# Optimization experiments

Hardware: AMD Instinct MI355X
Metric: run time of the kernel (lower is better)

The kernel has to match this reference:

```python
import jax, jax.numpy as jnp
import numpy as np

GAMMA = 1.0

def setup_inputs() -> dict:
    key = jax.random.key(0)
    kx, ky = jax.random.split(key)
    X = jax.random.normal(kx, (8192, 64), dtype=jnp.float32)
    Y = jax.random.normal(ky, (8192, 64), dtype=jnp.float32)
    return {"X": X, "Y": Y}

def reference(X, Y):
    x2 = jnp.sum(X * X, axis=-1)            # (n,)
    y2 = jnp.sum(Y * Y, axis=-1)            # (m,)
    xy = X @ Y.T                            # (n, m)
    dist2 = x2[:, None] + y2[None, :] - 2.0 * xy
    dist2 = jnp.maximum(dist2, 0.0)         # numerical guard
    return jnp.exp(-GAMMA * dist2)
```

## Files before the change

### kernel.cpp

```cpp
#include <hip/hip_runtime.h>

typedef __attribute__((ext_vector_type(8))) short          short8_t;
typedef __attribute__((ext_vector_type(8))) unsigned short ushort8_t;
typedef __attribute__((ext_vector_type(4))) float          floatx4;

constexpr int N_ROWS = 8192;
constexpr int DIM    = 64;
constexpr int PANEL  = 128 * DIM;

__device__ __forceinline__ unsigned short bf16_rne(float f) {
    unsigned int u = __float_as_uint(f);
    u += 0x7FFFu + ((u >> 16) & 1u);
    return (unsigned short)(u >> 16);
}

__global__ void __launch_bounds__(256)
split_norms_kernel(const float* __restrict__ X, const float* __restrict__ Y,
                   float* __restrict__ x2, float* __restrict__ y2,
                   unsigned short* __restrict__ Xs, unsigned short* __restrict__ Ys) {
    const int t  = blockIdx.x * 256 + threadIdx.x;
    const int r  = t >> 1;
    const int h  = t & 1;
    const int p  = r >> 7;
    const int rl = r & 127;
    const int g  = rl >> 4;
    const int li = rl & 15;
    const size_t pb = (size_t)p * (2 * PANEL);

    const float4* xr = reinterpret_cast<const float4*>(X + (size_t)r * DIM + h * 32);
    const float4* yr = reinterpret_cast<const float4*>(Y + (size_t)r * DIM + h * 32);

    float sx = 0.f, sy = 0.f;
#pragma unroll
    for (int c = 0; c < 4; ++c) {
        const int off = ((g * 2 + h) * 64 + c * 16 + li) * 8;
        float f[8];
        ushort8_t hi, lo;

        *reinterpret_cast<float4*>(&f[0]) = xr[2 * c];
        *reinterpret_cast<float4*>(&f[4]) = xr[2 * c + 1];
#pragma unroll
        for (int e = 0; e < 8; ++e) {
            sx = fmaf(f[e], f[e], sx);
            unsigned short hh = bf16_rne(f[e]);
            hi[e] = hh;
            lo[e] = bf16_rne(f[e] - __uint_as_float((unsigned int)hh << 16));
        }
        *reinterpret_cast<ushort8_t*>(&Xs[pb + off])         = hi;
        *reinterpret_cast<ushort8_t*>(&Xs[pb + PANEL + off]) = lo;

        *reinterpret_cast<float4*>(&f[0]) = yr[2 * c];
        *reinterpret_cast<float4*>(&f[4]) = yr[2 * c + 1];
#pragma unroll
        for (int e = 0; e < 8; ++e) {
            sy = fmaf(f[e], f[e], sy);
            unsigned short hh = bf16_rne(f[e]);
            hi[e] = hh;
            lo[e] = bf16_rne(f[e] - __uint_as_float((unsigned int)hh << 16));
        }
        *reinterpret_cast<ushort8_t*>(&Ys[pb + off])         = hi;
        *reinterpret_cast<ushort8_t*>(&Ys[pb + PANEL + off]) = lo;
    }
    sx += __shfl_xor(sx, 1);
    sy += __shfl_xor(sy, 1);
    if (h == 0) { x2[r] = sx; y2[r] = sy; }
}

__global__ void __launch_bounds__(64)
rbf_mfma_kernel(const unsigned short* __restrict__ Xs,
                const unsigned short* __restrict__ Ys,
                const float* __restrict__ x2, const float* __restrict__ y2,
                float* __restrict__ out) {
    const int lane = threadIdx.x;
    const int row0 = blockIdx.y * 64;
    const int col0 = blockIdx.x * 64;
    const unsigned short* Xp = Xs + (size_t)(blockIdx.y >> 1) * (2 * PANEL);
    const unsigned short* Yp = Ys + (size_t)(blockIdx.x >> 1) * (2 * PANEL);
    const int gx0 = (blockIdx.y & 1) * 4;
    const int gy0 = (blockIdx.x & 1) * 4;

    floatx4 acc[4][4] = {};

#define GF(P, hl, g, ks)                                                       \
    (*reinterpret_cast<const short8_t*>(                                       \
        (P) + (hl) * PANEL + (((g) * 2 + (ks)) * 64 + lane) * 8))

#pragma unroll
    for (int ks = 0; ks < 2; ++ks) {
        short8_t aH[4], bH[4], aL[4], bL[4];
#pragma unroll
        for (int mi = 0; mi < 4; ++mi) aH[mi] = GF(Xp, 0, gx0 + mi, ks);
#pragma unroll
        for (int ni = 0; ni < 4; ++ni) bH[ni] = GF(Yp, 0, gy0 + ni, ks);
#pragma unroll
        for (int mi = 0; mi < 4; ++mi)
#pragma unroll
            for (int ni = 0; ni < 4; ++ni)
                acc[mi][ni] = __builtin_amdgcn_mfma_f32_16x16x32_bf16(
                    bH[ni], aH[mi], acc[mi][ni], 0, 0, 0);
#pragma unroll
        for (int ni = 0; ni < 4; ++ni) bL[ni] = GF(Yp, 1, gy0 + ni, ks);
#pragma unroll
        for (int mi = 0; mi < 4; ++mi)
#pragma unroll
            for (int ni = 0; ni < 4; ++ni)
                acc[mi][ni] = __builtin_amdgcn_mfma_f32_16x16x32_bf16(
                    bL[ni], aH[mi], acc[mi][ni], 0, 0, 0);
#pragma unroll
        for (int mi = 0; mi < 4; ++mi) aL[mi] = GF(Xp, 1, gx0 + mi, ks);
#pragma unroll
        for (int mi = 0; mi < 4; ++mi)
#pragma unroll
            for (int ni = 0; ni < 4; ++ni)
                acc[mi][ni] = __builtin_amdgcn_mfma_f32_16x16x32_bf16(
                    bH[ni], aL[mi], acc[mi][ni], 0, 0, 0);
    }
#undef GF

    const int li = lane & 15;
    const int lg = lane >> 4;
    const int orow = row0 + li;
    const int ocol = col0 + lg * 4;
#pragma unroll
    for (int mi = 0; mi < 4; ++mi) {
        const float xs = x2[orow + mi * 16];
        float* obase = out + (size_t)(orow + mi * 16) * N_ROWS + ocol;
#pragma unroll
        for (int ni = 0; ni < 4; ++ni) {
            const float4 yv = *reinterpret_cast<const float4*>(&y2[ocol + ni * 16]);
            float4 o;
            o.x = __expf(-fmaxf(fmaf(-2.f, acc[mi][ni][0], xs + yv.x), 0.f));
            o.y = __expf(-fmaxf(fmaf(-2.f, acc[mi][ni][1], xs + yv.y), 0.f));
            o.z = __expf(-fmaxf(fmaf(-2.f, acc[mi][ni][2], xs + yv.z), 0.f));
            o.w = __expf(-fmaxf(fmaf(-2.f, acc[mi][ni][3], xs + yv.w), 0.f));
            *reinterpret_cast<float4*>(obase + ni * 16) = o;
        }
    }
}

extern "C" void kernel_launch(void* const* d_in, const int* in_sizes, int n_in,
                              void* d_out, int out_size, void* d_ws, size_t ws_size,
                              hipStream_t stream) {
    const float* X = (const float*)d_in[0];
    const float* Y = (const float*)d_in[1];
    float* out = (float*)d_out;

    float* x2 = (float*)d_ws;
    float* y2 = x2 + N_ROWS;
    unsigned short* Xs = (unsigned short*)(y2 + N_ROWS);
    unsigned short* Ys = Xs + (N_ROWS / 128) * 2 * PANEL;

    split_norms_kernel<<<(2 * N_ROWS) / 256, 256, 0, stream>>>(X, Y, x2, y2, Xs, Ys);

    dim3 grid(N_ROWS / 64, N_ROWS / 64);
    rbf_mfma_kernel<<<grid, 64, 0, stream>>>(Xs, Ys, x2, y2, out);
}
```

Baseline: 73.60 us.

## Persistent 256-thread blocks with register-resident X and LDS-transposed coalesced stores

Replaces the 16K single-wave blocks with 256 persistent blocks of four waves. Each wave keeps its 64-row X fragments in registers and loops over 16 column chunks of 64. Accumulators are staged through a per-wave swizzled LDS buffer so each output row is written as 256 contiguous bytes rather than scattered 16-byte pieces. This targets launch overhead, repeated X loads and store coalescing on a write-bound 256MB output. The trade-off is fewer blocks, which may limit latency hiding, plus LDS traffic and serialized per-chunk phases.

```diff
diff --git a/kernel.cpp b/kernel.cpp
--- a/kernel.cpp
+++ b/kernel.cpp
@@ -66,74 +66,98 @@
     if (h == 0) { x2[r] = sx; y2[r] = sy; }
 }
 
-__global__ void __launch_bounds__(64)
+__global__ void __launch_bounds__(256, 2)
 rbf_mfma_kernel(const unsigned short* __restrict__ Xs,
                 const unsigned short* __restrict__ Ys,
                 const float* __restrict__ x2, const float* __restrict__ y2,
                 float* __restrict__ out) {
-    const int lane = threadIdx.x;
-    const int row0 = blockIdx.y * 64;
-    const int col0 = blockIdx.x * 64;
-    const unsigned short* Xp = Xs + (size_t)(blockIdx.y >> 1) * (2 * PANEL);
-    const unsigned short* Yp = Ys + (size_t)(blockIdx.x >> 1) * (2 * PANEL);
-    const int gx0 = (blockIdx.y & 1) * 4;
-    const int gy0 = (blockIdx.x & 1) * 4;
+    __shared__ float4 Rbuf[4][1024];
 
-    floatx4 acc[4][4] = {};
+    const int tid  = threadIdx.x;
+    const int lane = tid & 63;
+    const int w    = tid >> 6;
+    const int li   = lane & 15;
+    const int lg   = lane >> 4;
 
-#define GF(P, hl, g, ks)                                                       \
-    (*reinterpret_cast<const short8_t*>(                                       \
-        (P) + (hl) * PANEL + (((g) * 2 + (ks)) * 64 + lane) * 8))
+    const int band = blockIdx.x & 31;
+    const int cq   = blockIdx.x >> 5;
+    const int row0 = band * 256 + w * 64;
+    const int colbase = cq * 1024;
+
+    short8_t aH[4][2], aL[4][2];
+    const int gx0 = row0 >> 4;
+#pragma unroll
+    for (int gx = 0; gx < 4; ++gx) {
+        const int gabs = gx0 + gx;
+        const unsigned short* base = Xs + (size_t)(gabs >> 3) * (2 * PANEL);
+        const int g = gabs & 7;
+#pragma unroll
+        for (int ks = 0; ks < 2; ++ks) {
+            const int off = ((g * 2 + ks) * 64 + lane) * 8;
+            aH[gx][ks] = *reinterpret_cast<const short8_t*>(base + off);
+            aL[gx][ks] = *reinterpret_cast<const short8_t*>(base + PANEL + off);
+        }
+    }
+
+    for (int ch = 0; ch < 16; ++ch) {
+        const int c0 = colbase + ch * 64;
+
+        short8_t bH[4][2], bL[4][2];
+        const int gy0 = c0 >> 4;
+#pragma unroll
+        for (int gy = 0; gy < 4; ++gy) {
+            const int gabs = gy0 + gy;
+            const unsigned short* base = Ys + (size_t)(gabs >> 3) * (2 * PANEL);
+            const int g = gabs & 7;
+#pragma unroll
+            for (int ks = 0; ks < 2; ++ks) {
+                const int off = ((g * 2 + ks) * 64 + lane) * 8;
+                bH[gy][ks] = *reinterpret_cast<const short8_t*>(base + off);
+                bL[gy][ks] = *reinterpret_cast<const short8_t*>(base + PANEL + off);
+            }
+        }
+
+        floatx4 acc[4][4] = {};
+#pragma unroll
+        for (int ks = 0; ks < 2; ++ks)
+#pragma unroll
+            for (int gy = 0; gy < 4; ++gy)
+#pragma unroll
+                for (int gx = 0; gx < 4; ++gx) {
+                    acc[gx][gy] = __builtin_amdgcn_mfma_f32_16x16x32_bf16(
+                        bH[gy][ks], aH[gx][ks], acc[gx][gy], 0, 0, 0);
+                    acc[gx][gy] = __builtin_amdgcn_mfma_f32_16x16x32_bf16(
+                        bL[gy][ks], aH[gx][ks], acc[gx][gy], 0, 0, 0);
+                    acc[gx][gy] = __builtin_amdgcn_mfma_f32_16x16x32_bf16(
+                        bH[gy][ks], aL[gx][ks], acc[gx][gy], 0, 0, 0);
+                }
 
 #pragma unroll
-    for (int ks = 0; ks < 2; ++ks) {
-        short8_t aH[4], bH[4], aL[4], bL[4];
+        for (int gx = 0; gx < 4; ++gx) {
+            const int row = gx * 16 + li;
 #pragma unroll
-        for (int mi = 0; mi < 4; ++mi) aH[mi] = GF(Xp, 0, gx0 + mi, ks);
+            for (int gy = 0; gy < 4; ++gy) {
+                const int cg = gy * 4 + lg;
+                Rbuf[w][row * 16 + (cg ^ (row & 7))] =
+                    make_float4(acc[gx][gy][0], acc[gx][gy][1],
+                                acc[gx][gy][2], acc[gx][gy][3]);
+            }
+        }
+        __builtin_amdgcn_s_waitcnt(0);
+
+        const float4 yv = *reinterpret_cast<const float4*>(&y2[c0 + li * 4]);
 #pragma unroll
-        for (int ni = 0; ni < 4; ++ni) bH[ni] = GF(Yp, 0, gy0 + ni, ks);
-#pragma unroll
-        for (int mi = 0; mi < 4; ++mi)
-#pragma unroll
-            for (int ni = 0; ni < 4; ++ni)
-                acc[mi][ni] = __builtin_amdgcn_mfma_f32_16x16x32_bf16(
-                    bH[ni], aH[mi], acc[mi][ni], 0, 0, 0);
-#pragma unroll
-        for (int ni = 0; ni < 4; ++ni) bL[ni] = GF(Yp, 1, gy0 + ni, ks);
-#pragma unroll
-        for (int mi = 0; mi < 4; ++mi)
-#pragma unroll
-            for (int ni = 0; ni < 4; ++ni)
-                acc[mi][ni] = __builtin_amdgcn_mfma_f32_16x16x32_bf16(
-                    bL[ni], aH[mi], acc[mi][ni], 0, 0, 0);
-#pragma unroll
-        for (int mi = 0; mi < 4; ++mi) aL[mi] = GF(Xp, 1, gx0 + mi, ks);
-#pragma unroll
-        for (int mi = 0; mi < 4; ++mi)
-#pragma unroll
-            for (int ni = 0; ni < 4; ++ni)
-                acc[mi][ni] = __builtin_amdgcn_mfma_f32_16x16x32_bf16(
-                    bH[ni], aL[mi], acc[mi][ni], 0, 0, 0);
-    }
-#undef GF
-
-    const int li = lane & 15;
-    const int lg = lane >> 4;
-    const int orow = row0 + li;
-    const int ocol = col0 + lg * 4;
-#pragma unroll
-    for (int mi = 0; mi < 4; ++mi) {
-        const float xs = x2[orow + mi * 16];
-        float* obase = out + (size_t)(orow + mi * 16) * N_ROWS + ocol;
-#pragma unroll
-        for (int ni = 0; ni < 4; ++ni) {
-            const float4 yv = *reinterpret_cast<const float4*>(&y2[ocol + ni * 16]);
+        for (int i = 0; i < 16; ++i) {
+            const int rr = i * 4 + lg;
+            const float4 v = Rbuf[w][rr * 16 + (li ^ (rr & 7))];
+            const int grow = row0 + rr;
+            const float xs = x2[grow];
             float4 o;
-            o.x = __expf(-fmaxf(fmaf(-2.f, acc[mi][ni][0], xs + yv.x), 0.f));
-            o.y = __expf(-fmaxf(fmaf(-2.f, acc[mi][ni][1], xs + yv.y), 0.f));
-            o.z = __expf(-fmaxf(fmaf(-2.f, acc[mi][ni][2], xs + yv.z), 0.f));
-            o.w = __expf(-fmaxf(fmaf(-2.f, acc[mi][ni][3], xs + yv.w), 0.f));
-            *reinterpret_cast<float4*>(obase + ni * 16) = o;
+            o.x = __expf(-fmaxf(fmaf(-2.f, v.x, xs + yv.x), 0.f));
+            o.y = __expf(-fmaxf(fmaf(-2.f, v.y, xs + yv.y), 0.f));
+            o.z = __expf(-fmaxf(fmaf(-2.f, v.z, xs + yv.z), 0.f));
+            o.w = __expf(-fmaxf(fmaf(-2.f, v.w, xs + yv.w), 0.f));
+            *reinterpret_cast<float4*>(out + (size_t)grow * N_ROWS + c0 + li * 4) = o;
         }
     }
 }
@@ -152,6 +176,5 @@
 
     split_norms_kernel<<<(2 * N_ROWS) / 256, 256, 0, stream>>>(X, Y, x2, y2, Xs, Ys);
 
-    dim3 grid(N_ROWS / 64, N_ROWS / 64);
-    rbf_mfma_kernel<<<grid, 64, 0, stream>>>(Xs, Ys, x2, y2, out);
+    rbf_mfma_kernel<<<256, 256, 0, stream>>>(Xs, Ys, x2, y2, out);
 }
```

Result: slower. 75.32 us (+2.3%).
